# Optimization experiments

Hardware: AMD Instinct MI355X
Metric: run time of the kernel (lower is better)

Reference implementation:

```python
import jax, jax.numpy as jnp
import numpy as np

N_HEADS = 16
K_CH = 1024 // N_HEADS  # 64
SCALE = 1.0 / np.sqrt(K_CH)


def setup_inputs() -> dict:
    key = jax.random.key(0)
    ks = jax.random.split(key, 10)
    B, C, T = 4, 1024, 2048
    Cout = 1024
    xavier = lambda k, o, i: jax.random.uniform(k, (o, i), jnp.float32, -1.0, 1.0) * np.sqrt(6.0 / (o + i))
    return {
        "x": jax.random.normal(ks[0], (B, C, T), jnp.float32),
        "c": jax.random.normal(ks[1], (B, C, T), jnp.float32),
        "Wq": xavier(ks[2], C, C), "bq": jnp.zeros((C,), jnp.float32),
        "Wk": xavier(ks[3], C, C), "bk": jnp.zeros((C,), jnp.float32),
        "Wv": xavier(ks[4], C, C), "bv": jnp.zeros((C,), jnp.float32),
        "Wo": xavier(ks[5], Cout, C), "bo": jnp.zeros((Cout,), jnp.float32),
    }


def reference(x, c, Wq, bq, Wk, bk, Wv, bv, Wo, bo):
    B, C, T = x.shape
    H, K = N_HEADS, K_CH
    # 1x1 Conv1d == per-timestep linear: [O,C] @ [B,C,T] -> [B,O,T]
    q = jnp.einsum('oc,bct->bot', Wq, x) + bq[None, :, None]
    k = jnp.einsum('oc,bct->bot', Wk, c) + bk[None, :, None]
    v = jnp.einsum('oc,bct->bot', Wv, c) + bv[None, :, None]
    # split heads: b (h k) t -> b h k t
    q = q.reshape(B, H, K, T)
    k = k.reshape(B, H, K, -1)
    v = v.reshape(B, H, K, -1)
    scores = jnp.einsum('bhkt,bhks->bhts', q, k) * SCALE  # [B,H,Tt,Ts]
    p = jax.nn.softmax(scores, axis=-1)
    out = jnp.einsum('bhts,bhks->bhkt', p, v)  # b h k t
    out = out.reshape(B, H * K, T)
    return jnp.einsum('oc,bct->bot', Wo, out) + bo[None, :, None]
```

## Files before the change

kernel.cpp:

```cpp
#include <hip/hip_runtime.h>
#include <stdint.h>

typedef __bf16 bf16x8 __attribute__((ext_vector_type(8)));
typedef float f32x4 __attribute__((ext_vector_type(4)));
typedef float f32x16 __attribute__((ext_vector_type(16)));
typedef unsigned u32x2 __attribute__((ext_vector_type(2)));
typedef unsigned u32x4 __attribute__((ext_vector_type(4)));

#define LOG2E 1.44269504088896340736f
#define ATT_SCALE 0.125f
#define CL (ATT_SCALE * LOG2E)
#define SWZ(row, colb) ((colb) ^ (((row) & 7) << 4))

#define GLOAD_LDS16(gp, lp)                                                  \
  __builtin_amdgcn_global_load_lds(                                          \
      (const __attribute__((address_space(1))) void*)(gp),                   \
      (__attribute__((address_space(3))) void*)(lp), 16, 0, 0)

__device__ __forceinline__ unsigned short f2bf(float f) {
  unsigned int x = __float_as_uint(f);
  x += 0x7fffu + ((x >> 16) & 1u);
  return (unsigned short)(x >> 16);
}

__device__ __forceinline__ float fexp2(float x) {
#if __has_builtin(__builtin_amdgcn_exp2f)
  return __builtin_amdgcn_exp2f(x);
#else
  return exp2f(x);
#endif
}

__device__ __forceinline__ unsigned cvtpk(float lo, float hi) {
  unsigned r;
  asm("v_cvt_pk_bf16_f32 %0, %1, %2" : "=v"(r) : "v"(lo), "v"(hi));
  return r;
}

__device__ __forceinline__ u32x2 plswap(unsigned a, unsigned b) {
#if __has_builtin(__builtin_amdgcn_permlane32_swap)
  return __builtin_amdgcn_permlane32_swap(a, b, false, false);
#else
  unsigned ax = (unsigned)__shfl_xor((int)a, 32);
  unsigned bx = (unsigned)__shfl_xor((int)b, 32);
  int hi = (threadIdx.x & 32) ? 1 : 0;
  u32x2 r;
  r[0] = hi ? bx : a;
  r[1] = hi ? b : ax;
  return r;
#endif
}

__global__ __launch_bounds__(256) void cvt_weights(
    const float* __restrict__ w0, const float* __restrict__ w1,
    const float* __restrict__ w2, const float* __restrict__ w3,
    unsigned short* __restrict__ o0, unsigned short* __restrict__ o1,
    unsigned short* __restrict__ o2, unsigned short* __restrict__ o3) {
  int sel = blockIdx.x >> 10;
  const float* in = sel == 0 ? w0 : sel == 1 ? w1 : sel == 2 ? w2 : w3;
  unsigned short* out = sel == 0 ? o0 : sel == 1 ? o1 : sel == 2 ? o2 : o3;
  float scale = sel == 0 ? CL : 1.0f;
  int i = ((blockIdx.x & 1023) * 256 + threadIdx.x) * 4;
  float4 v = *(const float4*)(in + i);
  ushort4 o;
  o.x = f2bf(v.x * scale); o.y = f2bf(v.y * scale);
  o.z = f2bf(v.z * scale); o.w = f2bf(v.w * scale);
  *(ushort4*)(out + i) = o;
}

__global__ __launch_bounds__(256) void transpose_cvt2(const float* __restrict__ x,
                                                      const float* __restrict__ c,
                                                      unsigned short* __restrict__ xT,
                                                      unsigned short* __restrict__ cT) {
  __shared__ unsigned short tile[32][33];
  const int C = 1024, T = 2048;
  int z = blockIdx.z;
  const float* in = (z < 4) ? x : c;
  unsigned short* out = (z < 4) ? xT : cT;
  int b = z & 3;
  int t0 = blockIdx.x * 32, c0 = blockIdx.y * 32;
  int tx = threadIdx.x & 31, ty = threadIdx.x >> 5;
  const float* src = in + ((size_t)b * C + c0) * T + t0;
  #pragma unroll
  for (int i = 0; i < 4; ++i) {
    int cc = ty + i * 8;
    tile[cc][tx] = f2bf(src[(size_t)cc * T + tx]);
  }
  __syncthreads();
  unsigned short* dst = out + ((size_t)b * T + t0) * C + c0;
  #pragma unroll
  for (int i = 0; i < 4; ++i) {
    int tt = ty + i * 8;
    dst[(size_t)tt * C + tx] = tile[tx][tt];
  }
}

__global__ __launch_bounds__(256) void qkv_gemm(
    const unsigned short* __restrict__ xT, const unsigned short* __restrict__ cT,
    const unsigned short* __restrict__ wq, const unsigned short* __restrict__ wk,
    const unsigned short* __restrict__ wv,
    const float* __restrict__ bq, const float* __restrict__ bk,
    const float* __restrict__ bv,
    unsigned short* __restrict__ QT, unsigned short* __restrict__ KT,
    unsigned short* __restrict__ Vb) {
  __shared__ __align__(16) char lds[2][32768];
  const size_t sBT = (size_t)2048 * 1024;

  const int id = (blockIdx.x & 7) * 192 + (blockIdx.x >> 3);
  const int op = id >> 9;
  const int r = id & 511;
  const int z = r >> 7;
  const unsigned short *A, *Bw;
  unsigned short* Cp;
  const float* bias;
  int m0, n0, ldC, bias_is_m;
  float bs;
  if (op == 2) {
    n0 = (r & 15) * 128; m0 = ((r >> 4) & 7) * 128;
    A = wv; Bw = cT + z * sBT; Cp = Vb + z * (size_t)1024 * 2048;
    bias = bv; ldC = 2048; bias_is_m = 1; bs = 1.0f;
  } else {
    n0 = (r & 7) * 128; m0 = ((r >> 3) & 15) * 128;
    A = (op == 0 ? xT : cT) + z * sBT;
    Bw = (op == 0 ? wq : wk);
    Cp = (op == 0 ? QT : KT) + z * sBT;
    bias = (op == 0 ? bq : bk); ldC = 1024; bias_is_m = 0;
    bs = (op == 0) ? CL : 1.0f;
  }

  const int tid = threadIdx.x;
  const int l = tid & 63, w = tid >> 6;
  const int g = l >> 4, j = l & 15;
  const int wr = w >> 1, wc = w & 1;
  const int srow = tid >> 3, sslot = tid & 7;

  f32x4 acc[4][4] = {};

  auto stage = [&](int bsel, int k0) {
    char* As = lds[bsel];
    char* Bs = lds[bsel] + 16384;
    #pragma unroll
    for (int p = 0; p < 4; ++p) {
      int row = p * 32 + srow;
      int ch = sslot ^ (row & 7);
      GLOAD_LDS16(A + (size_t)(m0 + row) * 1024 + k0 + ch * 8, As + (p * 256 + tid) * 16);
      GLOAD_LDS16(Bw + (size_t)(n0 + row) * 1024 + k0 + ch * 8, Bs + (p * 256 + tid) * 16);
    }
  };

  stage(0, 0);
  __syncthreads();

  for (int t = 0; t < 16; ++t) {
    int cur = t & 1;
    if (t < 15) stage(cur ^ 1, (t + 1) * 64);
    char* As = lds[cur];
    char* Bs = lds[cur] + 16384;
    #pragma unroll
    for (int k2 = 0; k2 < 2; ++k2) {
      bf16x8 af[4], bfr[4];
      #pragma unroll
      for (int mf = 0; mf < 4; ++mf) {
        int row = wr * 64 + mf * 16 + j;
        af[mf] = *(const bf16x8*)(As + row * 128 + SWZ(row, k2 * 64 + g * 16));
      }
      #pragma unroll
      for (int nf = 0; nf < 4; ++nf) {
        int row = wc * 64 + nf * 16 + j;
        bfr[nf] = *(const bf16x8*)(Bs + row * 128 + SWZ(row, k2 * 64 + g * 16));
      }
      #pragma unroll
      for (int mf = 0; mf < 4; ++mf)
        #pragma unroll
        for (int nf = 0; nf < 4; ++nf)
          acc[mf][nf] = __builtin_amdgcn_mfma_f32_16x16x32_bf16(af[mf], bfr[nf], acc[mf][nf], 0, 0, 0);
    }
    __syncthreads();
  }

  #pragma unroll
  for (int mf = 0; mf < 4; ++mf) {
    #pragma unroll
    for (int rr = 0; rr < 4; ++rr) {
      int m = m0 + wr * 64 + mf * 16 + g * 4 + rr;
      float bm = bias_is_m ? bias[m] * bs : 0.f;
      #pragma unroll
      for (int nf = 0; nf < 4; ++nf) {
        int n = n0 + wc * 64 + nf * 16 + j;
        float val = acc[mf][nf][rr] + bm + (bias_is_m ? 0.f : bias[n] * bs);
        Cp[(size_t)m * ldC + n] = f2bf(val);
      }
    }
  }
}

__global__ __launch_bounds__(256) void gemm_out(
    const unsigned short* __restrict__ Wo, const unsigned short* __restrict__ OT,
    float* __restrict__ Out, const float* __restrict__ bias) {
  __shared__ __align__(16) char lds[2][32768];
  const size_t sBT = (size_t)2048 * 1024;
  const int z = blockIdx.z;
  const int m0 = blockIdx.y * 128, n0 = blockIdx.x * 128;
  const unsigned short* A = Wo;
  const unsigned short* B = OT + z * sBT;
  float* Cp = Out + z * (size_t)1024 * 2048;

  const int tid = threadIdx.x;
  const int l = tid & 63, w = tid >> 6;
  const int g = l >> 4, j = l & 15;
  const int wr = w >> 1, wc = w & 1;
  const int srow = tid >> 3, sslot = tid & 7;

  f32x4 acc[4][4] = {};

  auto stage = [&](int bsel, int k0) {
    char* As = lds[bsel];
    char* Bs = lds[bsel] + 16384;
    #pragma unroll
    for (int p = 0; p < 4; ++p) {
      int row = p * 32 + srow;
      int ch = sslot ^ (row & 7);
      GLOAD_LDS16(A + (size_t)(m0 + row) * 1024 + k0 + ch * 8, As + (p * 256 + tid) * 16);
      GLOAD_LDS16(B + (size_t)(n0 + row) * 1024 + k0 + ch * 8, Bs + (p * 256 + tid) * 16);
    }
  };

  stage(0, 0);
  __syncthreads();

  for (int t = 0; t < 16; ++t) {
    int cur = t & 1;
    if (t < 15) stage(cur ^ 1, (t + 1) * 64);
    char* As = lds[cur];
    char* Bs = lds[cur] + 16384;
    #pragma unroll
    for (int k2 = 0; k2 < 2; ++k2) {
      bf16x8 af[4], bfr[4];
      #pragma unroll
      for (int mf = 0; mf < 4; ++mf) {
        int row = wr * 64 + mf * 16 + j;
        af[mf] = *(const bf16x8*)(As + row * 128 + SWZ(row, k2 * 64 + g * 16));
      }
      #pragma unroll
      for (int nf = 0; nf < 4; ++nf) {
        int row = wc * 64 + nf * 16 + j;
        bfr[nf] = *(const bf16x8*)(Bs + row * 128 + SWZ(row, k2 * 64 + g * 16));
      }
      #pragma unroll
      for (int mf = 0; mf < 4; ++mf)
        #pragma unroll
        for (int nf = 0; nf < 4; ++nf)
          acc[mf][nf] = __builtin_amdgcn_mfma_f32_16x16x32_bf16(af[mf], bfr[nf], acc[mf][nf], 0, 0, 0);
    }
    __syncthreads();
  }

  #pragma unroll
  for (int mf = 0; mf < 4; ++mf) {
    #pragma unroll
    for (int rr = 0; rr < 4; ++rr) {
      int m = m0 + wr * 64 + mf * 16 + g * 4 + rr;
      float bm = bias[m];
      #pragma unroll
      for (int nf = 0; nf < 4; ++nf) {
        int n = n0 + wc * 64 + nf * 16 + j;
        Cp[(size_t)m * 2048 + n] = acc[mf][nf][rr] + bm;
      }
    }
  }
}

__global__ __launch_bounds__(256, 3) void attn_kernel4(const unsigned short* __restrict__ QT,
                                                       const unsigned short* __restrict__ KT,
                                                       const unsigned short* __restrict__ V,
                                                       unsigned short* __restrict__ OT) {
  __shared__ __align__(16) char kv[2][16384];
  __shared__ float lbuf[4][32];

  const int fid = blockIdx.x;
  const int xcd = fid & 7, idx = fid >> 3;
  const int bh = ((idx & 7) << 3) | xcd;
  const int tblk = idx >> 3;
  const int b = bh >> 4, h = bh & 15;

  const int tid = threadIdx.x;
  const int w = tid >> 6, l = tid & 63, lo5 = l & 31, hi = l >> 5;
  const int tq0 = tblk * 128 + w * 32;

  bf16x8 q[4];
  {
    const unsigned short* Qb = QT + ((size_t)(b * 2048 + tq0 + lo5)) * 1024 + h * 64 + hi * 8;
    #pragma unroll
    for (int kb = 0; kb < 4; ++kb) q[kb] = *(const bf16x8*)(Qb + kb * 16);
  }

  f32x16 o[2] = {};
  float lr = 0.f;

  const int srow0 = tid >> 3, sslot = tid & 7;
  const unsigned short* Kg0 = KT + ((size_t)b * 2048) * 1024 + h * 64;
  const unsigned short* Vg0 = V + ((size_t)(b * 1024 + h * 64)) * 2048;

  auto stage = [&](int bsel, int s0) {
    char* Ks = kv[bsel];
    char* Vs = kv[bsel] + 8192;
    #pragma unroll
    for (int p = 0; p < 2; ++p) {
      int row = p * 32 + srow0;
      int ch = sslot ^ (row & 7);
      GLOAD_LDS16(Kg0 + (size_t)(s0 + row) * 1024 + ch * 8, Ks + (p * 256 + tid) * 16);
      GLOAD_LDS16(Vg0 + (size_t)row * 2048 + s0 + ch * 8, Vs + (p * 256 + tid) * 16);
    }
  };

  stage(0, 0);
  __syncthreads();

  for (int t = 0; t < 32; ++t) {
    int cur = t & 1;
    if (t < 31) stage(cur ^ 1, (t + 1) * 64);
    char* Ks = kv[cur];
    char* Vs = kv[cur] + 8192;

    f32x16 p0 = {}, p1 = {};
    #pragma unroll
    for (int kb = 0; kb < 4; ++kb) {
      int r0 = lo5, r1 = 32 + lo5;
      bf16x8 ka0 = *(const bf16x8*)(Ks + r0 * 128 + SWZ(r0, kb * 32 + hi * 16));
      bf16x8 ka1 = *(const bf16x8*)(Ks + r1 * 128 + SWZ(r1, kb * 32 + hi * 16));
      p0 = __builtin_amdgcn_mfma_f32_32x32x16_bf16(ka0, q[kb], p0, 0, 0, 0);
      p1 = __builtin_amdgcn_mfma_f32_32x32x16_bf16(ka1, q[kb], p1, 0, 0, 0);
    }

    float ls0 = 0.f, ls1 = 0.f, ls2 = 0.f, ls3 = 0.f;
    #pragma unroll
    for (int r = 0; r < 16; r += 4) {
      float e0 = fexp2(p0[r]), e1 = fexp2(p0[r + 1]), e2 = fexp2(p0[r + 2]), e3 = fexp2(p0[r + 3]);
      p0[r] = e0; p0[r + 1] = e1; p0[r + 2] = e2; p0[r + 3] = e3;
      ls0 += e0; ls1 += e1; ls2 += e2; ls3 += e3;
    }
    #pragma unroll
    for (int r = 0; r < 16; r += 4) {
      float e0 = fexp2(p1[r]), e1 = fexp2(p1[r + 1]), e2 = fexp2(p1[r + 2]), e3 = fexp2(p1[r + 3]);
      p1[r] = e0; p1[r + 1] = e1; p1[r + 2] = e2; p1[r + 3] = e3;
      ls0 += e0; ls1 += e1; ls2 += e2; ls3 += e3;
    }
    lr += (ls0 + ls1) + (ls2 + ls3);

    u32x4 pa[4];
    {
      u32x2 ra = plswap(cvtpk(p0[0], p0[1]), cvtpk(p0[4], p0[5]));
      u32x2 rb = plswap(cvtpk(p0[2], p0[3]), cvtpk(p0[6], p0[7]));
      pa[0] = (u32x4){ra[0], rb[0], ra[1], rb[1]};
      u32x2 rc = plswap(cvtpk(p0[8], p0[9]), cvtpk(p0[12], p0[13]));
      u32x2 rd = plswap(cvtpk(p0[10], p0[11]), cvtpk(p0[14], p0[15]));
      pa[1] = (u32x4){rc[0], rd[0], rc[1], rd[1]};
      u32x2 re = plswap(cvtpk(p1[0], p1[1]), cvtpk(p1[4], p1[5]));
      u32x2 rf = plswap(cvtpk(p1[2], p1[3]), cvtpk(p1[6], p1[7]));
      pa[2] = (u32x4){re[0], rf[0], re[1], rf[1]};
      u32x2 rg = plswap(cvtpk(p1[8], p1[9]), cvtpk(p1[12], p1[13]));
      u32x2 rh = plswap(cvtpk(p1[10], p1[11]), cvtpk(p1[14], p1[15]));
      pa[3] = (u32x4){rg[0], rh[0], rg[1], rh[1]};
    }

    #pragma unroll
    for (int sb = 0; sb < 4; ++sb)
      #pragma unroll
      for (int kb2 = 0; kb2 < 2; ++kb2) {
        int row = kb2 * 32 + lo5;
        bf16x8 vb = *(const bf16x8*)(Vs + row * 128 + SWZ(row, sb * 32 + hi * 16));
        o[kb2] = __builtin_amdgcn_mfma_f32_32x32x16_bf16(
            __builtin_bit_cast(bf16x8, pa[sb]), vb, o[kb2], 0, 0, 0);
      }
    __syncthreads();
  }

  u32x2 sw = plswap(__float_as_uint(lr), __float_as_uint(lr));
  float lt = __uint_as_float(sw[0]) + __uint_as_float(sw[1]);
  if (hi == 0) lbuf[w][lo5] = 1.0f / lt;
  unsigned short* Ob = OT + ((size_t)(b * 2048 + tq0)) * 1024 + h * 64 + lo5;
  #pragma unroll
  for (int r = 0; r < 16; ++r) {
    int srow = (r & 3) + 8 * (r >> 2) + 4 * hi;
    float inv = lbuf[w][srow];
    Ob[(size_t)srow * 1024 + 0]  = f2bf(o[0][r] * inv);
    Ob[(size_t)srow * 1024 + 32] = f2bf(o[1][r] * inv);
  }
}

extern "C" void kernel_launch(void* const* d_in, const int* in_sizes, int n_in,
                              void* d_out, int out_size, void* d_ws, size_t ws_size,
                              hipStream_t stream) {
  const float* x  = (const float*)d_in[0];
  const float* c  = (const float*)d_in[1];
  const float* Wq = (const float*)d_in[2];
  const float* bq = (const float*)d_in[3];
  const float* Wk = (const float*)d_in[4];
  const float* bk = (const float*)d_in[5];
  const float* Wv = (const float*)d_in[6];
  const float* bv = (const float*)d_in[7];
  const float* Wo = (const float*)d_in[8];
  const float* bo = (const float*)d_in[9];

  const size_t MB = 1024 * 1024;
  char* ws = (char*)d_ws;
  unsigned short* wqb = (unsigned short*)(ws + 0 * MB);
  unsigned short* wkb = (unsigned short*)(ws + 2 * MB);
  unsigned short* wvb = (unsigned short*)(ws + 4 * MB);
  unsigned short* wob = (unsigned short*)(ws + 6 * MB);
  unsigned short* xT  = (unsigned short*)(ws + 8 * MB);
  unsigned short* cT  = (unsigned short*)(ws + 24 * MB);
  unsigned short* QT  = (unsigned short*)(ws + 40 * MB);
  unsigned short* KT  = (unsigned short*)(ws + 56 * MB);
  unsigned short* Vb  = (unsigned short*)(ws + 72 * MB);
  unsigned short* OT  = xT;

  cvt_weights<<<dim3(4096), 256, 0, stream>>>(Wq, Wk, Wv, Wo, wqb, wkb, wvb, wob);
  transpose_cvt2<<<dim3(64, 32, 8), 256, 0, stream>>>(x, c, xT, cT);

  qkv_gemm<<<dim3(1536), 256, 0, stream>>>(xT, cT, wqb, wkb, wvb, bq, bk, bv, QT, KT, Vb);

  attn_kernel4<<<dim3(1024), 256, 0, stream>>>(QT, KT, Vb, OT);

  gemm_out<<<dim3(16, 8, 4), 256, 0, stream>>>(wob, OT, (float*)d_out, bo);
}
```

Before: 205.8 us.

## Enlarge QKV GEMM tiles to 256x256 with 8-wave ping-pong pipeline

Rewrites the fused QKV projection GEMM to use 256x256 output tiles with 512-thread blocks (8 waves, each computing 128x64), cutting the grid from 1536 to 384 blocks. The K loop is split into four phases that interleave LDS fragment reads, staggered async global-to-LDS prefetch of the A and B halves, barriers and s_setprio-raised MFMA bursts. The aim is more operand reuse per loaded byte and better overlap of memory traffic with matrix math. In exchange it uses 128KB of LDS per block and more accumulator registers, and 384 blocks may leave some CUs idle or cause a tail.

```diff
diff --git a/kernel.cpp b/kernel.cpp
--- a/kernel.cpp
+++ b/kernel.cpp
@@ -95,7 +95,7 @@
   }
 }
 
-__global__ __launch_bounds__(256) void qkv_gemm(
+__global__ __launch_bounds__(512, 2) void qkv_gemm8(
     const unsigned short* __restrict__ xT, const unsigned short* __restrict__ cT,
     const unsigned short* __restrict__ wq, const unsigned short* __restrict__ wk,
     const unsigned short* __restrict__ wv,
@@ -103,24 +103,26 @@
     const float* __restrict__ bv,
     unsigned short* __restrict__ QT, unsigned short* __restrict__ KT,
     unsigned short* __restrict__ Vb) {
-  __shared__ __align__(16) char lds[2][32768];
+  __shared__ __align__(16) char lds[131072];
   const size_t sBT = (size_t)2048 * 1024;
 
-  const int id = (blockIdx.x & 7) * 192 + (blockIdx.x >> 3);
-  const int op = id >> 9;
-  const int r = id & 511;
-  const int z = r >> 7;
+  const int bid = blockIdx.x;
+  const int id = (bid & 7) * 48 + (bid >> 3);
+  const int op = id >> 7;
+  const int r = id & 127;
+  const int z = r >> 5, tt = r & 31;
+
   const unsigned short *A, *Bw;
   unsigned short* Cp;
   const float* bias;
   int m0, n0, ldC, bias_is_m;
   float bs;
   if (op == 2) {
-    n0 = (r & 15) * 128; m0 = ((r >> 4) & 7) * 128;
+    m0 = (tt & 3) * 256; n0 = (tt >> 2) * 256;
     A = wv; Bw = cT + z * sBT; Cp = Vb + z * (size_t)1024 * 2048;
     bias = bv; ldC = 2048; bias_is_m = 1; bs = 1.0f;
   } else {
-    n0 = (r & 7) * 128; m0 = ((r >> 3) & 15) * 128;
+    m0 = (tt >> 2) * 256; n0 = (tt & 3) * 256;
     A = (op == 0 ? xT : cT) + z * sBT;
     Bw = (op == 0 ? wq : wk);
     Cp = (op == 0 ? QT : KT) + z * sBT;
@@ -131,58 +133,135 @@
   const int tid = threadIdx.x;
   const int l = tid & 63, w = tid >> 6;
   const int g = l >> 4, j = l & 15;
-  const int wr = w >> 1, wc = w & 1;
+  const int wr = w >> 2, wc = w & 3;
   const int srow = tid >> 3, sslot = tid & 7;
 
-  f32x4 acc[4][4] = {};
-
-  auto stage = [&](int bsel, int k0) {
-    char* As = lds[bsel];
-    char* Bs = lds[bsel] + 16384;
-    #pragma unroll
-    for (int p = 0; p < 4; ++p) {
-      int row = p * 32 + srow;
-      int ch = sslot ^ (row & 7);
-      GLOAD_LDS16(A + (size_t)(m0 + row) * 1024 + k0 + ch * 8, As + (p * 256 + tid) * 16);
-      GLOAD_LDS16(Bw + (size_t)(n0 + row) * 1024 + k0 + ch * 8, Bs + (p * 256 + tid) * 16);
-    }
-  };
-
-  stage(0, 0);
-  __syncthreads();
-
-  for (int t = 0; t < 16; ++t) {
-    int cur = t & 1;
-    if (t < 15) stage(cur ^ 1, (t + 1) * 64);
-    char* As = lds[cur];
-    char* Bs = lds[cur] + 16384;
-    #pragma unroll
-    for (int k2 = 0; k2 < 2; ++k2) {
-      bf16x8 af[4], bfr[4];
-      #pragma unroll
-      for (int mf = 0; mf < 4; ++mf) {
-        int row = wr * 64 + mf * 16 + j;
-        af[mf] = *(const bf16x8*)(As + row * 128 + SWZ(row, k2 * 64 + g * 16));
-      }
-      #pragma unroll
-      for (int nf = 0; nf < 4; ++nf) {
-        int row = wc * 64 + nf * 16 + j;
-        bfr[nf] = *(const bf16x8*)(Bs + row * 128 + SWZ(row, k2 * 64 + g * 16));
-      }
-      #pragma unroll
-      for (int mf = 0; mf < 4; ++mf)
+  const unsigned short* ga[4];
+  const unsigned short* gb[4];
+  #pragma unroll
+  for (int c2 = 0; c2 < 4; ++c2) {
+    int ra = m0 + c2 * 64 + srow;
+    ga[c2] = A + (size_t)ra * 1024 + (sslot ^ (ra & 7)) * 8;
+    int rb = n0 + c2 * 64 + srow;
+    gb[c2] = Bw + (size_t)rb * 1024 + (sslot ^ (rb & 7)) * 8;
+  }
+
+  f32x4 acc[8][4] = {};
+
+  {
+    char* As = lds;
+    char* Bs = lds + 32768;
+    #pragma unroll
+    for (int c2 = 0; c2 < 4; ++c2) {
+      GLOAD_LDS16(ga[c2], As + c2 * 8192 + tid * 16);
+      GLOAD_LDS16(gb[c2], Bs + c2 * 8192 + tid * 16);
+      ga[c2] += 64; gb[c2] += 64;
+    }
+  }
+  asm volatile("s_waitcnt vmcnt(0)" ::: "memory");
+  __builtin_amdgcn_s_barrier();
+
+  for (int kt = 0; kt < 16; ++kt) {
+    char* As = lds + (kt & 1) * 65536;
+    char* Bs = As + 32768;
+    char* An = lds + ((kt & 1) ^ 1) * 65536;
+    char* Bn = An + 32768;
+    const bool pf = (kt < 15);
+
+    bf16x8 af[4][2], bfr[4][2];
+
+    #pragma unroll
+    for (int mf = 0; mf < 4; ++mf) {
+      int row = wr * 128 + mf * 16 + j;
+      af[mf][0] = *(const bf16x8*)(As + row * 128 + SWZ(row, g * 16));
+      af[mf][1] = *(const bf16x8*)(As + row * 128 + SWZ(row, 64 + g * 16));
+    }
+    #pragma unroll
+    for (int nf = 0; nf < 2; ++nf) {
+      int row = wc * 64 + nf * 16 + j;
+      bfr[nf][0] = *(const bf16x8*)(Bs + row * 128 + SWZ(row, g * 16));
+      bfr[nf][1] = *(const bf16x8*)(Bs + row * 128 + SWZ(row, 64 + g * 16));
+    }
+    if (pf) {
+      #pragma unroll
+      for (int c2 = 0; c2 < 4; ++c2) {
+        GLOAD_LDS16(ga[c2], An + c2 * 8192 + tid * 16);
+        ga[c2] += 64;
+      }
+    }
+    __builtin_amdgcn_s_barrier();
+    __builtin_amdgcn_s_setprio(1);
+    #pragma unroll
+    for (int mf = 0; mf < 4; ++mf)
+      #pragma unroll
+      for (int nf = 0; nf < 2; ++nf)
         #pragma unroll
-        for (int nf = 0; nf < 4; ++nf)
-          acc[mf][nf] = __builtin_amdgcn_mfma_f32_16x16x32_bf16(af[mf], bfr[nf], acc[mf][nf], 0, 0, 0);
-    }
-    __syncthreads();
+        for (int k2 = 0; k2 < 2; ++k2)
+          acc[mf][nf] = __builtin_amdgcn_mfma_f32_16x16x32_bf16(af[mf][k2], bfr[nf][k2], acc[mf][nf], 0, 0, 0);
+    __builtin_amdgcn_s_setprio(0);
+    __builtin_amdgcn_s_barrier();
+
+    #pragma unroll
+    for (int nf = 2; nf < 4; ++nf) {
+      int row = wc * 64 + nf * 16 + j;
+      bfr[nf][0] = *(const bf16x8*)(Bs + row * 128 + SWZ(row, g * 16));
+      bfr[nf][1] = *(const bf16x8*)(Bs + row * 128 + SWZ(row, 64 + g * 16));
+    }
+    if (pf) {
+      #pragma unroll
+      for (int c2 = 0; c2 < 4; ++c2) {
+        GLOAD_LDS16(gb[c2], Bn + c2 * 8192 + tid * 16);
+        gb[c2] += 64;
+      }
+    }
+    __builtin_amdgcn_s_barrier();
+    __builtin_amdgcn_s_setprio(1);
+    #pragma unroll
+    for (int mf = 0; mf < 4; ++mf)
+      #pragma unroll
+      for (int nf = 2; nf < 4; ++nf)
+        #pragma unroll
+        for (int k2 = 0; k2 < 2; ++k2)
+          acc[mf][nf] = __builtin_amdgcn_mfma_f32_16x16x32_bf16(af[mf][k2], bfr[nf][k2], acc[mf][nf], 0, 0, 0);
+    __builtin_amdgcn_s_setprio(0);
+    __builtin_amdgcn_s_barrier();
+
+    #pragma unroll
+    for (int mf = 0; mf < 4; ++mf) {
+      int row = wr * 128 + (mf + 4) * 16 + j;
+      af[mf][0] = *(const bf16x8*)(As + row * 128 + SWZ(row, g * 16));
+      af[mf][1] = *(const bf16x8*)(As + row * 128 + SWZ(row, 64 + g * 16));
+    }
+    __builtin_amdgcn_s_barrier();
+    __builtin_amdgcn_s_setprio(1);
+    #pragma unroll
+    for (int mf = 0; mf < 4; ++mf)
+      #pragma unroll
+      for (int nf = 0; nf < 2; ++nf)
+        #pragma unroll
+        for (int k2 = 0; k2 < 2; ++k2)
+          acc[mf + 4][nf] = __builtin_amdgcn_mfma_f32_16x16x32_bf16(af[mf][k2], bfr[nf][k2], acc[mf + 4][nf], 0, 0, 0);
+    __builtin_amdgcn_s_setprio(0);
+    __builtin_amdgcn_s_barrier();
+
+    __builtin_amdgcn_s_setprio(1);
+    #pragma unroll
+    for (int mf = 0; mf < 4; ++mf)
+      #pragma unroll
+      for (int nf = 2; nf < 4; ++nf)
+        #pragma unroll
+        for (int k2 = 0; k2 < 2; ++k2)
+          acc[mf + 4][nf] = __builtin_amdgcn_mfma_f32_16x16x32_bf16(af[mf][k2], bfr[nf][k2], acc[mf + 4][nf], 0, 0, 0);
+    __builtin_amdgcn_s_setprio(0);
+    asm volatile("s_waitcnt vmcnt(0)" ::: "memory");
+    __builtin_amdgcn_s_barrier();
   }
 
   #pragma unroll
-  for (int mf = 0; mf < 4; ++mf) {
+  for (int mf = 0; mf < 8; ++mf) {
     #pragma unroll
     for (int rr = 0; rr < 4; ++rr) {
-      int m = m0 + wr * 64 + mf * 16 + g * 4 + rr;
+      int m = m0 + wr * 128 + mf * 16 + g * 4 + rr;
       float bm = bias_is_m ? bias[m] * bs : 0.f;
       #pragma unroll
       for (int nf = 0; nf < 4; ++nf) {
@@ -418,7 +497,7 @@
   cvt_weights<<<dim3(4096), 256, 0, stream>>>(Wq, Wk, Wv, Wo, wqb, wkb, wvb, wob);
   transpose_cvt2<<<dim3(64, 32, 8), 256, 0, stream>>>(x, c, xT, cT);
 
-  qkv_gemm<<<dim3(1536), 256, 0, stream>>>(xT, cT, wqb, wkb, wvb, bq, bk, bv, QT, KT, Vb);
+  qkv_gemm8<<<dim3(384), 512, 0, stream>>>(xT, cT, wqb, wkb, wvb, bq, bk, bv, QT, KT, Vb);
 
   attn_kernel4<<<dim3(1024), 256, 0, stream>>>(QT, KT, Vb, OT);
 
```

Result: slower. 214.8 us (+4.4%).

## Use triple-buffered K=32 GEMM core with explicit vmcnt waits and XCD block remap

Applied to the files above, without the earlier changes.

Replaces the double-buffered K=64 GEMM loops in the QKV and output projections with a shared templated core. The core uses three 16KB LDS stages of K=32, waits with s_waitcnt vmcnt plus a raw barrier, and keeps two loads in flight while cutting LDS per block to 48KB so three blocks fit per CU. The output GEMM also gets a 1D grid with an XCD-aware block remap for L2 locality. The risk is twice as many barriers per tile and a more intricate swizzle layout, where a mistake would corrupt results.

```diff
diff --git a/kernel.cpp b/kernel.cpp
--- a/kernel.cpp
+++ b/kernel.cpp
@@ -95,7 +95,92 @@
   }
 }
 
-__global__ __launch_bounds__(256) void qkv_gemm(
+template <int NT, int OUT_F32>
+__device__ __forceinline__ void gemm_core128(
+    const unsigned short* __restrict__ A, const unsigned short* __restrict__ B,
+    void* __restrict__ Cv, const float* __restrict__ bias, int bias_is_m,
+    float bs, int m0, int n0, int ldC) {
+  __shared__ __align__(16) char lds[3 * 16384];
+  const int tid = threadIdx.x;
+  const int l = tid & 63, w = tid >> 6;
+  const int g = l >> 4, j = l & 15;
+  const int wr = w >> 1, wc = w & 1;
+
+  const int r0 = tid >> 3;
+  const int slotp = (tid & 7) ^ (r0 & 7);
+  const int mloc = r0 * 2 + (slotp >> 2);
+  const int kg = slotp & 3;
+  const unsigned short* ga0 = A + (size_t)(m0 + mloc) * 1024 + kg * 8;
+  const unsigned short* ga1 = A + (size_t)(m0 + 64 + mloc) * 1024 + kg * 8;
+  const unsigned short* gb0 = B + (size_t)(n0 + mloc) * 1024 + kg * 8;
+  const unsigned short* gb1 = B + (size_t)(n0 + 64 + mloc) * 1024 + kg * 8;
+
+  auto stage = [&](char* buf) {
+    GLOAD_LDS16(ga0, buf + tid * 16);
+    GLOAD_LDS16(ga1, buf + 4096 + tid * 16);
+    GLOAD_LDS16(gb0, buf + 8192 + tid * 16);
+    GLOAD_LDS16(gb1, buf + 12288 + tid * 16);
+    ga0 += 32; ga1 += 32; gb0 += 32; gb1 += 32;
+  };
+
+  f32x4 acc[4][4] = {};
+
+  stage(lds);
+  stage(lds + 16384);
+
+  char* bufc = lds;
+  char* bufs = lds + 2 * 16384;
+
+  for (int t = 0; t < NT; ++t) {
+    if (t == NT - 1) asm volatile("s_waitcnt vmcnt(0)" ::: "memory");
+    else             asm volatile("s_waitcnt vmcnt(4)" ::: "memory");
+    __builtin_amdgcn_s_barrier();
+    asm volatile("" ::: "memory");
+    if (t < NT - 2) stage(bufs);
+
+    bf16x8 af[4], bfr[4];
+    #pragma unroll
+    for (int mf = 0; mf < 4; ++mf) {
+      int m = wr * 64 + mf * 16 + j;
+      int rp = m >> 1;
+      int cb = ((m & 1) * 64 + g * 16) ^ ((rp & 7) << 4);
+      af[mf] = *(const bf16x8*)(bufc + rp * 128 + cb);
+    }
+    #pragma unroll
+    for (int nf = 0; nf < 4; ++nf) {
+      int n = wc * 64 + nf * 16 + j;
+      int rp = n >> 1;
+      int cb = ((n & 1) * 64 + g * 16) ^ ((rp & 7) << 4);
+      bfr[nf] = *(const bf16x8*)(bufc + 8192 + rp * 128 + cb);
+    }
+    #pragma unroll
+    for (int mf = 0; mf < 4; ++mf)
+      #pragma unroll
+      for (int nf = 0; nf < 4; ++nf)
+        acc[mf][nf] = __builtin_amdgcn_mfma_f32_16x16x32_bf16(af[mf], bfr[nf], acc[mf][nf], 0, 0, 0);
+
+    bufc += 16384; if (bufc == lds + 49152) bufc = lds;
+    bufs += 16384; if (bufs == lds + 49152) bufs = lds;
+  }
+
+  #pragma unroll
+  for (int mf = 0; mf < 4; ++mf) {
+    #pragma unroll
+    for (int rr = 0; rr < 4; ++rr) {
+      int m = m0 + wr * 64 + mf * 16 + g * 4 + rr;
+      float bm = bias_is_m ? bias[m] * bs : 0.f;
+      #pragma unroll
+      for (int nf = 0; nf < 4; ++nf) {
+        int n = n0 + wc * 64 + nf * 16 + j;
+        float val = acc[mf][nf][rr] + bm + (bias_is_m ? 0.f : bias[n] * bs);
+        if (OUT_F32) ((float*)Cv)[(size_t)m * ldC + n] = val;
+        else ((unsigned short*)Cv)[(size_t)m * ldC + n] = f2bf(val);
+      }
+    }
+  }
+}
+
+__global__ __launch_bounds__(256, 3) void qkv_gemm3(
     const unsigned short* __restrict__ xT, const unsigned short* __restrict__ cT,
     const unsigned short* __restrict__ wq, const unsigned short* __restrict__ wk,
     const unsigned short* __restrict__ wv,
@@ -103,171 +188,40 @@
     const float* __restrict__ bv,
     unsigned short* __restrict__ QT, unsigned short* __restrict__ KT,
     unsigned short* __restrict__ Vb) {
-  __shared__ __align__(16) char lds[2][32768];
   const size_t sBT = (size_t)2048 * 1024;
-
   const int id = (blockIdx.x & 7) * 192 + (blockIdx.x >> 3);
   const int op = id >> 9;
   const int r = id & 511;
   const int z = r >> 7;
-  const unsigned short *A, *Bw;
+  const unsigned short *A, *B;
   unsigned short* Cp;
   const float* bias;
   int m0, n0, ldC, bias_is_m;
   float bs;
   if (op == 2) {
     n0 = (r & 15) * 128; m0 = ((r >> 4) & 7) * 128;
-    A = wv; Bw = cT + z * sBT; Cp = Vb + z * (size_t)1024 * 2048;
+    A = wv; B = cT + z * sBT; Cp = Vb + z * (size_t)1024 * 2048;
     bias = bv; ldC = 2048; bias_is_m = 1; bs = 1.0f;
   } else {
     n0 = (r & 7) * 128; m0 = ((r >> 3) & 15) * 128;
     A = (op == 0 ? xT : cT) + z * sBT;
-    Bw = (op == 0 ? wq : wk);
+    B = (op == 0 ? wq : wk);
     Cp = (op == 0 ? QT : KT) + z * sBT;
     bias = (op == 0 ? bq : bk); ldC = 1024; bias_is_m = 0;
     bs = (op == 0) ? CL : 1.0f;
   }
-
-  const int tid = threadIdx.x;
-  const int l = tid & 63, w = tid >> 6;
-  const int g = l >> 4, j = l & 15;
-  const int wr = w >> 1, wc = w & 1;
-  const int srow = tid >> 3, sslot = tid & 7;
-
-  f32x4 acc[4][4] = {};
-
-  auto stage = [&](int bsel, int k0) {
-    char* As = lds[bsel];
-    char* Bs = lds[bsel] + 16384;
-    #pragma unroll
-    for (int p = 0; p < 4; ++p) {
-      int row = p * 32 + srow;
-      int ch = sslot ^ (row & 7);
-      GLOAD_LDS16(A + (size_t)(m0 + row) * 1024 + k0 + ch * 8, As + (p * 256 + tid) * 16);
-      GLOAD_LDS16(Bw + (size_t)(n0 + row) * 1024 + k0 + ch * 8, Bs + (p * 256 + tid) * 16);
-    }
-  };
-
-  stage(0, 0);
-  __syncthreads();
-
-  for (int t = 0; t < 16; ++t) {
-    int cur = t & 1;
-    if (t < 15) stage(cur ^ 1, (t + 1) * 64);
-    char* As = lds[cur];
-    char* Bs = lds[cur] + 16384;
-    #pragma unroll
-    for (int k2 = 0; k2 < 2; ++k2) {
-      bf16x8 af[4], bfr[4];
-      #pragma unroll
-      for (int mf = 0; mf < 4; ++mf) {
-        int row = wr * 64 + mf * 16 + j;
-        af[mf] = *(const bf16x8*)(As + row * 128 + SWZ(row, k2 * 64 + g * 16));
-      }
-      #pragma unroll
-      for (int nf = 0; nf < 4; ++nf) {
-        int row = wc * 64 + nf * 16 + j;
-        bfr[nf] = *(const bf16x8*)(Bs + row * 128 + SWZ(row, k2 * 64 + g * 16));
-      }
-      #pragma unroll
-      for (int mf = 0; mf < 4; ++mf)
-        #pragma unroll
-        for (int nf = 0; nf < 4; ++nf)
-          acc[mf][nf] = __builtin_amdgcn_mfma_f32_16x16x32_bf16(af[mf], bfr[nf], acc[mf][nf], 0, 0, 0);
-    }
-    __syncthreads();
-  }
-
-  #pragma unroll
-  for (int mf = 0; mf < 4; ++mf) {
-    #pragma unroll
-    for (int rr = 0; rr < 4; ++rr) {
-      int m = m0 + wr * 64 + mf * 16 + g * 4 + rr;
-      float bm = bias_is_m ? bias[m] * bs : 0.f;
-      #pragma unroll
-      for (int nf = 0; nf < 4; ++nf) {
-        int n = n0 + wc * 64 + nf * 16 + j;
-        float val = acc[mf][nf][rr] + bm + (bias_is_m ? 0.f : bias[n] * bs);
-        Cp[(size_t)m * ldC + n] = f2bf(val);
-      }
-    }
-  }
-}
-
-__global__ __launch_bounds__(256) void gemm_out(
+  gemm_core128<32, 0>(A, B, Cp, bias, bias_is_m, bs, m0, n0, ldC);
+}
+
+__global__ __launch_bounds__(256, 3) void gemm_out3(
     const unsigned short* __restrict__ Wo, const unsigned short* __restrict__ OT,
     float* __restrict__ Out, const float* __restrict__ bias) {
-  __shared__ __align__(16) char lds[2][32768];
   const size_t sBT = (size_t)2048 * 1024;
-  const int z = blockIdx.z;
-  const int m0 = blockIdx.y * 128, n0 = blockIdx.x * 128;
-  const unsigned short* A = Wo;
-  const unsigned short* B = OT + z * sBT;
-  float* Cp = Out + z * (size_t)1024 * 2048;
-
-  const int tid = threadIdx.x;
-  const int l = tid & 63, w = tid >> 6;
-  const int g = l >> 4, j = l & 15;
-  const int wr = w >> 1, wc = w & 1;
-  const int srow = tid >> 3, sslot = tid & 7;
-
-  f32x4 acc[4][4] = {};
-
-  auto stage = [&](int bsel, int k0) {
-    char* As = lds[bsel];
-    char* Bs = lds[bsel] + 16384;
-    #pragma unroll
-    for (int p = 0; p < 4; ++p) {
-      int row = p * 32 + srow;
-      int ch = sslot ^ (row & 7);
-      GLOAD_LDS16(A + (size_t)(m0 + row) * 1024 + k0 + ch * 8, As + (p * 256 + tid) * 16);
-      GLOAD_LDS16(B + (size_t)(n0 + row) * 1024 + k0 + ch * 8, Bs + (p * 256 + tid) * 16);
-    }
-  };
-
-  stage(0, 0);
-  __syncthreads();
-
-  for (int t = 0; t < 16; ++t) {
-    int cur = t & 1;
-    if (t < 15) stage(cur ^ 1, (t + 1) * 64);
-    char* As = lds[cur];
-    char* Bs = lds[cur] + 16384;
-    #pragma unroll
-    for (int k2 = 0; k2 < 2; ++k2) {
-      bf16x8 af[4], bfr[4];
-      #pragma unroll
-      for (int mf = 0; mf < 4; ++mf) {
-        int row = wr * 64 + mf * 16 + j;
-        af[mf] = *(const bf16x8*)(As + row * 128 + SWZ(row, k2 * 64 + g * 16));
-      }
-      #pragma unroll
-      for (int nf = 0; nf < 4; ++nf) {
-        int row = wc * 64 + nf * 16 + j;
-        bfr[nf] = *(const bf16x8*)(Bs + row * 128 + SWZ(row, k2 * 64 + g * 16));
-      }
-      #pragma unroll
-      for (int mf = 0; mf < 4; ++mf)
-        #pragma unroll
-        for (int nf = 0; nf < 4; ++nf)
-          acc[mf][nf] = __builtin_amdgcn_mfma_f32_16x16x32_bf16(af[mf], bfr[nf], acc[mf][nf], 0, 0, 0);
-    }
-    __syncthreads();
-  }
-
-  #pragma unroll
-  for (int mf = 0; mf < 4; ++mf) {
-    #pragma unroll
-    for (int rr = 0; rr < 4; ++rr) {
-      int m = m0 + wr * 64 + mf * 16 + g * 4 + rr;
-      float bm = bias[m];
-      #pragma unroll
-      for (int nf = 0; nf < 4; ++nf) {
-        int n = n0 + wc * 64 + nf * 16 + j;
-        Cp[(size_t)m * 2048 + n] = acc[mf][nf][rr] + bm;
-      }
-    }
-  }
+  const int id = (blockIdx.x & 7) * 64 + (blockIdx.x >> 3);
+  const int z = id >> 7;
+  const int m0 = ((id >> 4) & 7) * 128, n0 = (id & 15) * 128;
+  gemm_core128<32, 1>(Wo, OT + z * sBT, Out + z * (size_t)1024 * 2048,
+                      bias, 1, 1.0f, m0, n0, 2048);
 }
 
 __global__ __launch_bounds__(256, 3) void attn_kernel4(const unsigned short* __restrict__ QT,
@@ -418,9 +372,9 @@
   cvt_weights<<<dim3(4096), 256, 0, stream>>>(Wq, Wk, Wv, Wo, wqb, wkb, wvb, wob);
   transpose_cvt2<<<dim3(64, 32, 8), 256, 0, stream>>>(x, c, xT, cT);
 
-  qkv_gemm<<<dim3(1536), 256, 0, stream>>>(xT, cT, wqb, wkb, wvb, bq, bk, bv, QT, KT, Vb);
+  qkv_gemm3<<<dim3(1536), 256, 0, stream>>>(xT, cT, wqb, wkb, wvb, bq, bk, bv, QT, KT, Vb);
 
   attn_kernel4<<<dim3(1024), 256, 0, stream>>>(QT, KT, Vb, OT);
 
-  gemm_out<<<dim3(16, 8, 4), 256, 0, stream>>>(wob, OT, (float*)d_out, bo);
-}
+  gemm_out3<<<dim3(512), 256, 0, stream>>>(wob, OT, (float*)d_out, bo);
+}
```

Result: faster. 196.2 us (-4.6%).
